# Kernel optimization log

Hardware: AMD Instinct MI355X
Metric: run time of the kernel (lower is better)

The kernel has to match this reference:

```python
import jax, jax.numpy as jnp
import numpy as np

CHUNK = 128


def selective_scan(x, A, Bm, Cm, dt, chunk_size):
    # x: [B,L,H,hd], Bm/Cm: [B,L,H,ds], A/dt: [H]. L must be divisible by chunk_size.
    Bb, L, H, hd = x.shape
    ds = Bm.shape[-1]
    cs = chunk_size
    nc = L // cs
    decay = jnp.exp(A * dt)  # [H]
    x_c = x.reshape(Bb, nc, cs, H, hd).transpose(0, 1, 3, 2, 4)   # [B,nc,H,cs,hd]
    B_c = Bm.reshape(Bb, nc, cs, H, ds).transpose(0, 1, 3, 2, 4)  # [B,nc,H,cs,ds]
    C_c = Cm.reshape(Bb, nc, cs, H, ds).transpose(0, 1, 3, 2, 4)
    x_dt = x_c * dt[None, None, :, None, None]
    idx = jnp.arange(cs, dtype=x.dtype)
    diff = idx[:, None] - idx[None, :]
    # causal intra-chunk decay matrix [H,cs,cs]
    L_mat = jnp.where(diff >= 0, decay[:, None, None] ** jnp.maximum(diff, 0.0), 0.0)
    CB = jnp.einsum('bnhid,bnhjd->bnhij', C_c, B_c)          # [B,nc,H,cs,cs]
    y_diag = jnp.einsum('bnhij,bnhjd->bnhid', CB * L_mat[None, None], x_dt)
    rev = jnp.arange(cs - 1, -1, -1, dtype=x.dtype)
    decay_rev = decay[:, None] ** rev[None, :]               # [H,cs]
    B_w = B_c * decay_rev[None, None, :, :, None]
    states = jnp.einsum('bnhjs,bnhjd->bnhsd', B_w, x_dt)     # [B,nc,H,ds,hd]
    cidx = jnp.arange(nc, dtype=x.dtype)
    shift = cidx[:, None] - cidx[None, :] - 1.0
    chunk_decay = decay ** cs
    M = jnp.where(shift >= 0, chunk_decay[:, None, None] ** jnp.maximum(shift, 0.0), 0.0)  # [H,nc,nc]
    h_carry = jnp.einsum('hij,bjhsd->bihsd', M, states)      # [B,nc,H,ds,hd]
    decay_out = decay[:, None] ** (idx[None, :] + 1.0)       # [H,cs]
    y_off = jnp.einsum('bnhis,bnhsd->bnhid', C_c, h_carry) * decay_out[None, None, :, :, None]
    y = (y_diag + y_off).transpose(0, 1, 3, 2, 4).reshape(Bb, L, H, hd)
    return y


def setup_inputs() -> dict:
    key = jax.random.key(0)
    ks = jax.random.split(key, 9)
    B, L, d_model, d_inner, H, ds, K = 2, 4096, 1024, 2048, 16, 128, 4
    s_dm = 1.0 / np.sqrt(d_model)
    s_di = 1.0 / np.sqrt(d_inner)
    x = jax.random.normal(ks[0], (B, L, d_model), jnp.float32)
    x_prenorm = jax.random.normal(ks[1], (B, L, d_model), jnp.float32)
    in_proj_w = jax.random.normal(ks[2], (2 * d_inner, d_model), jnp.float32) * s_dm
    conv_w = jax.random.normal(ks[3], (d_inner, 1, K), jnp.float32) * 0.5
    conv_b = jax.random.normal(ks[4], (d_inner,), jnp.float32) * 0.01
    B_proj_w = jax.random.normal(ks[5], (H * ds, d_model), jnp.float32) * s_dm
    C_proj_w = jax.random.normal(ks[6], (H * ds, d_model), jnp.float32) * s_dm
    dt_init = jax.random.uniform(ks[7], (H,), jnp.float32, 0.001, 0.1)
    dt_bias = dt_init + jnp.log(-jnp.expm1(-dt_init))  # inverse softplus
    A_log = jnp.log(jnp.arange(1, H + 1, dtype=jnp.float32))
    D_param = jnp.ones((H,), jnp.float32)
    out_proj_w = jax.random.normal(ks[8], (d_model, d_inner), jnp.float32) * s_di
    return dict(x=x, x_prenorm=x_prenorm, in_proj_w=in_proj_w, conv_w=conv_w,
                conv_b=conv_b, B_proj_w=B_proj_w, C_proj_w=C_proj_w,
                dt_bias=dt_bias, A_log=A_log, D_param=D_param, out_proj_w=out_proj_w)


def reference(x, x_prenorm, in_proj_w, conv_w, conv_b, B_proj_w, C_proj_w,
              dt_bias, A_log, D_param, out_proj_w):
    Bb, L, d_model = x.shape
    H = A_log.shape[0]
    ds = B_proj_w.shape[0] // H
    vg = x @ in_proj_w.T                        # [B,L,2*d_inner]
    d_inner = vg.shape[-1] // 2
    value, gate = vg[..., :d_inner], vg[..., d_inner:]
    K = conv_w.shape[-1]
    # causal depthwise conv1d (torch pads K-1 both sides then truncates right)
    v = jax.lax.conv_general_dilated(
        value.transpose(0, 2, 1), conv_w, (1,), [(K - 1, 0)],
        feature_group_count=d_inner, dimension_numbers=('NCH', 'OIH', 'NCH'))
    v = v + conv_b[None, :, None]
    value = jax.nn.silu(v.transpose(0, 2, 1))   # [B,L,d_inner]
    Bm = (x_prenorm @ B_proj_w.T).reshape(Bb, L, H, ds)
    Cm = (x_prenorm @ C_proj_w.T).reshape(Bb, L, H, ds)
    dt = jax.nn.softplus(dt_bias)
    A = -jnp.exp(A_log)
    hd = d_inner // H
    vh = value.reshape(Bb, L, H, hd)
    y = selective_scan(vh, A, Bm, Cm, dt, CHUNK)
    y = y + D_param[None, None, :, None] * vh
    y = y.reshape(Bb, L, d_inner) * jax.nn.silu(gate)
    return y @ out_proj_w.T
```

## Files before the change

kernel.cpp:

```cpp
#include <hip/hip_runtime.h>
#include <hip/hip_bf16.h>

#define NB 2
#define LSEQ 4096
#define DM 1024
#define DI 2048
#define NH 16
#define DSZ 128
#define CS 128
#define NCHUNK 32

using bf16 = __hip_bfloat16;
typedef __attribute__((ext_vector_type(8))) short short8;
typedef __attribute__((ext_vector_type(4))) float f32x4;

__device__ __forceinline__ float b2f(unsigned short u) {
    union { unsigned i; float f; } c; c.i = ((unsigned)u) << 16; return c.f;
}
__device__ __forceinline__ bf16 f2bf(float v) { return __float2bfloat16(v); }
__device__ __forceinline__ float bf2f(bf16 v) { return __bfloat162float(v); }

__device__ __forceinline__ float head_dt(const float* dt_bias, int h) {
    return log1pf(expf(dt_bias[h]));
}
__device__ __forceinline__ float head_l2dec(const float* dt_bias, const float* A_log, int h, float* dt_out) {
    float dt = head_dt(dt_bias, h);
    *dt_out = dt;
    return -expf(A_log[h]) * dt * 1.4426950408889634f;
}

__device__ __forceinline__ void storeC(bf16* C, size_t idx, float v) { C[idx] = f2bf(v); }
__device__ __forceinline__ void storeC(float* C, size_t idx, float v) { C[idx] = v; }

__device__ __forceinline__ void gload16(const bf16* g, bf16* l) {
    __builtin_amdgcn_global_load_lds(
        (const __attribute__((address_space(1))) void*)g,
        (__attribute__((address_space(3))) void*)l, 16, 0, 0);
}

__global__ __launch_bounds__(256) void cast_f2b(const float* __restrict__ in,
                                                bf16* __restrict__ out, long n) {
    long i = ((long)blockIdx.x * 256 + threadIdx.x) * 8;
    if (i >= n) return;
    float4 a = *reinterpret_cast<const float4*>(in + i);
    float4 b = *reinterpret_cast<const float4*>(in + i + 4);
    union { bf16 h[8]; short8 v; } o;
    o.h[0] = f2bf(a.x); o.h[1] = f2bf(a.y); o.h[2] = f2bf(a.z); o.h[3] = f2bf(a.w);
    o.h[4] = f2bf(b.x); o.h[5] = f2bf(b.y); o.h[6] = f2bf(b.z); o.h[7] = f2bf(b.w);
    *reinterpret_cast<short8*>(out + i) = o.v;
}

template <int MODE, typename TO>
__global__ __launch_bounds__(256) void gemm_mfma(const bf16* __restrict__ A,
                                                 const bf16* __restrict__ W,
                                                 TO* __restrict__ C0, TO* __restrict__ C1,
                                                 int N, int K) {
    __shared__ bf16 As[2][128 * 32];
    __shared__ bf16 Ws[2][128 * 32];
    const int tid = threadIdx.x;
    const int lane = tid & 63, w = tid >> 6;
    const int wr = w >> 1, wc = w & 1;
    const int bm = blockIdx.y * 128, bn = blockIdx.x * 128;
    const int srow = lane >> 2;
    const int skoff = (((lane & 3) ^ ((lane >> 2) & 3)) * 8);
    const int g0 = w * 2, g1 = w * 2 + 1;
    const int fr = lane & 15;
    const int fk = (((lane >> 4) ^ (lane & 3)) * 8);
    f32x4 acc[4][4] = {};
#define STAGE(buf, kt)                                                                  \
    do {                                                                                \
        gload16(A + (size_t)(bm + g0 * 16 + srow) * K + (kt) + skoff, &As[buf][g0 * 512]); \
        gload16(A + (size_t)(bm + g1 * 16 + srow) * K + (kt) + skoff, &As[buf][g1 * 512]); \
        gload16(W + (size_t)(bn + g0 * 16 + srow) * K + (kt) + skoff, &Ws[buf][g0 * 512]); \
        gload16(W + (size_t)(bn + g1 * 16 + srow) * K + (kt) + skoff, &Ws[buf][g1 * 512]); \
    } while (0)
    STAGE(0, 0);
    __syncthreads();
    const int NT = K / 32;
    int cur = 0;
    for (int t = 0; t < NT; ++t) {
        if (t + 1 < NT) STAGE(cur ^ 1, (t + 1) * 32);
        short8 af[4], bfr[4];
#pragma unroll
        for (int mi = 0; mi < 4; ++mi)
            af[mi] = *reinterpret_cast<const short8*>(&As[cur][(wr * 64 + mi * 16 + fr) * 32 + fk]);
#pragma unroll
        for (int ni = 0; ni < 4; ++ni)
            bfr[ni] = *reinterpret_cast<const short8*>(&Ws[cur][(wc * 64 + ni * 16 + fr) * 32 + fk]);
#pragma unroll
        for (int mi = 0; mi < 4; ++mi)
#pragma unroll
            for (int ni = 0; ni < 4; ++ni)
                acc[mi][ni] = __builtin_amdgcn_mfma_f32_16x16x32_bf16(af[mi], bfr[ni], acc[mi][ni], 0, 0, 0);
        __syncthreads();
        cur ^= 1;
    }
#undef STAGE
    const int orow0 = (lane >> 4) * 4;
    const int ocol = lane & 15;
#pragma unroll
    for (int mi = 0; mi < 4; ++mi)
#pragma unroll
        for (int ni = 0; ni < 4; ++ni) {
            int col = bn + wc * 64 + ni * 16 + ocol;
#pragma unroll
            for (int r = 0; r < 4; ++r) {
                int row = bm + wr * 64 + mi * 16 + orow0 + r;
                float v = acc[mi][ni][r];
                if (MODE == 1) {
                    if (col < DI) storeC(C0, (size_t)row * DI + col, v);
                    else          storeC(C1, (size_t)row * DI + (col - DI), v);
                } else {
                    storeC(C0, (size_t)row * N + col, v);
                }
            }
        }
}

__global__ __launch_bounds__(256) void conv_silu_vec(const bf16* __restrict__ vpre,
                                                     const float* __restrict__ cw,
                                                     const float* __restrict__ cb,
                                                     bf16* __restrict__ vpost) {
    size_t e = ((size_t)blockIdx.x * 256 + threadIdx.x) * 8;
    int c = (int)(e & (DI - 1));
    size_t bl = e >> 11;
    int l = (int)(bl & (LSEQ - 1));
    float vin[4][8];
#pragma unroll
    for (int k = 0; k < 4; ++k) {
        if (l - 3 + k >= 0) {
            short8 v = *reinterpret_cast<const short8*>(vpre + e + (long)(k - 3) * DI);
#pragma unroll
            for (int j = 0; j < 8; ++j) vin[k][j] = b2f((unsigned short)v[j]);
        } else {
#pragma unroll
            for (int j = 0; j < 8; ++j) vin[k][j] = 0.f;
        }
    }
    union { bf16 h[8]; short8 v; } o;
#pragma unroll
    for (int j = 0; j < 8; ++j) {
        float4 w4 = *reinterpret_cast<const float4*>(cw + (c + j) * 4);
        float s = cb[c + j] + w4.x * vin[0][j] + w4.y * vin[1][j] + w4.z * vin[2][j] + w4.w * vin[3][j];
        o.h[j] = f2bf(s / (1.f + expf(-s)));
    }
    *reinterpret_cast<short8*>(vpost + e) = o.v;
}

template <int SCALEMODE>
__global__ __launch_bounds__(256) void transpose_chunk(const bf16* __restrict__ in, bf16* __restrict__ outp,
                                                       const float* __restrict__ dt_bias,
                                                       const float* __restrict__ A_log) {
    __shared__ bf16 Ts[128][136];
    __shared__ float dpow[128];
    const int tid = threadIdx.x;
    const int bid = blockIdx.x;
    const int h = bid & 15, bn = bid >> 4;
    float dt; float l2d = head_l2dec(dt_bias, A_log, h, &dt);
    if (SCALEMODE == 1 && tid < 128) dpow[tid] = exp2f((float)(127 - tid) * l2d);
    const size_t base = (size_t)bn * CS * 2048 + (size_t)h * 128;
    {
        const int jr = tid >> 4, c8 = (tid & 15) * 8;
        for (int j0 = 0; j0 < 128; j0 += 16)
            *reinterpret_cast<short8*>(&Ts[j0 + jr][c8]) =
                *reinterpret_cast<const short8*>(in + base + (size_t)(j0 + jr) * 2048 + c8);
    }
    __syncthreads();
    const size_t ob = (size_t)bid * 16384;
    const int d = tid & 127;
    for (int jg = (tid >> 7); jg < 16; jg += 2) {
        int j0 = jg * 8;
        union { bf16 h8[8]; short8 v; } o;
#pragma unroll
        for (int e = 0; e < 8; ++e) {
            float val = bf2f(Ts[j0 + e][d]);
            val *= (SCALEMODE == 1) ? dpow[j0 + e] : dt;
            o.h8[e] = f2bf(val);
        }
        *reinterpret_cast<short8*>(outp + ob + (size_t)d * 128 + j0) = o.v;
    }
}

__global__ __launch_bounds__(256) void chunk_statesT(const bf16* __restrict__ XDT,
                                                     const bf16* __restrict__ BTg,
                                                     bf16* __restrict__ STT) {
    __shared__ bf16 XTs[128][72];
    __shared__ bf16 BTs[128][72];
    const int tid = threadIdx.x;
    const size_t ob = (size_t)blockIdx.x * 16384;
    const int lane = tid & 63, w = tid >> 6;
    const int fr = lane & 15, fk = (lane >> 4) * 8;
    f32x4 acc[2][8] = {};
    for (int j0 = 0; j0 < 128; j0 += 64) {
        for (int rr = 0; rr < 128; rr += 32) {
            int row = rr + (tid >> 3);
            int col = (tid & 7) * 8;
            *reinterpret_cast<short8*>(&XTs[row][col]) =
                *reinterpret_cast<const short8*>(XDT + ob + (size_t)row * 128 + j0 + col);
            *reinterpret_cast<short8*>(&BTs[row][col]) =
                *reinterpret_cast<const short8*>(BTg + ob + (size_t)row * 128 + j0 + col);
        }
        __syncthreads();
#pragma unroll
        for (int ks = 0; ks < 2; ++ks) {
            short8 a[2], bfr[8];
#pragma unroll
            for (int mi = 0; mi < 2; ++mi)
                a[mi] = *reinterpret_cast<const short8*>(&XTs[w * 32 + mi * 16 + fr][ks * 32 + fk]);
#pragma unroll
            for (int ni = 0; ni < 8; ++ni)
                bfr[ni] = *reinterpret_cast<const short8*>(&BTs[ni * 16 + fr][ks * 32 + fk]);
#pragma unroll
            for (int mi = 0; mi < 2; ++mi)
#pragma unroll
                for (int ni = 0; ni < 8; ++ni)
                    acc[mi][ni] = __builtin_amdgcn_mfma_f32_16x16x32_bf16(a[mi], bfr[ni], acc[mi][ni], 0, 0, 0);
        }
        __syncthreads();
    }
    const int orow0 = (lane >> 4) * 4, ocol = lane & 15;
#pragma unroll
    for (int mi = 0; mi < 2; ++mi)
#pragma unroll
        for (int ni = 0; ni < 8; ++ni) {
            int s = ni * 16 + ocol;
#pragma unroll
            for (int r = 0; r < 4; ++r) {
                int d = w * 32 + mi * 16 + orow0 + r;
                STT[ob + (size_t)d * 128 + s] = f2bf(acc[mi][ni][r]);
            }
        }
}

__global__ __launch_bounds__(256) void scan_kernel(bf16* __restrict__ ST,
                                                   const float* __restrict__ dt_bias,
                                                   const float* __restrict__ A_log) {
    const int q = blockIdx.x & 7;
    const int h = (blockIdx.x >> 3) & 15;
    const int b = blockIdx.x >> 7;
    float dt; float l2d = head_l2dec(dt_bias, A_log, h, &dt);
    float cd = exp2f(128.f * l2d);
    const int tid = threadIdx.x;
    float r[8] = {};
    for (int n = 0; n < NCHUNK; ++n) {
        size_t base = ((size_t)((b * NCHUNK + n) * NH + h)) * 16384 + (size_t)q * 2048;
#pragma unroll
        for (int e = 0; e < 8; ++e) {
            size_t idx = base + e * 256 + tid;
            float v = bf2f(ST[idx]);
            ST[idx] = f2bf(r[e]);
            r[e] = cd * r[e] + v;
        }
    }
}

__global__ __launch_bounds__(256) void chunk_cbl_mfma(const bf16* __restrict__ Bm, const bf16* __restrict__ Cm,
                                                      const float* __restrict__ dt_bias,
                                                      const float* __restrict__ A_log,
                                                      bf16* __restrict__ P) {
    __shared__ bf16 Cs[128][72];
    __shared__ bf16 Bs[128][72];
    const int tid = threadIdx.x;
    const int bid = blockIdx.x;
    const int h = bid & 15, bn = bid >> 4;
    float dt; float l2d = head_l2dec(dt_bias, A_log, h, &dt);
    const size_t base = (size_t)bn * CS * 2048 + (size_t)h * 128;
    const int lane = tid & 63, w = tid >> 6;
    const int fr = lane & 15, fk = (lane >> 4) * 8;
    f32x4 acc[2][8] = {};
    for (int s0 = 0; s0 < 128; s0 += 64) {
        for (int rr = 0; rr < 128; rr += 32) {
            int row = rr + (tid >> 3);
            int col = (tid & 7) * 8;
            *reinterpret_cast<short8*>(&Cs[row][col]) =
                *reinterpret_cast<const short8*>(Cm + base + (size_t)row * 2048 + s0 + col);
            *reinterpret_cast<short8*>(&Bs[row][col]) =
                *reinterpret_cast<const short8*>(Bm + base + (size_t)row * 2048 + s0 + col);
        }
        __syncthreads();
#pragma unroll
        for (int ks = 0; ks < 2; ++ks) {
            short8 a[2], bfr[8];
#pragma unroll
            for (int mi = 0; mi < 2; ++mi)
                a[mi] = *reinterpret_cast<const short8*>(&Cs[w * 32 + mi * 16 + fr][ks * 32 + fk]);
#pragma unroll
            for (int ni = 0; ni < 8; ++ni)
                bfr[ni] = *reinterpret_cast<const short8*>(&Bs[ni * 16 + fr][ks * 32 + fk]);
#pragma unroll
            for (int mi = 0; mi < 2; ++mi)
#pragma unroll
                for (int ni = 0; ni < 8; ++ni)
                    acc[mi][ni] = __builtin_amdgcn_mfma_f32_16x16x32_bf16(a[mi], bfr[ni], acc[mi][ni], 0, 0, 0);
        }
        __syncthreads();
    }
    const size_t ob = (size_t)bid * 16384;
    const int orow0 = (lane >> 4) * 4, ocol = lane & 15;
#pragma unroll
    for (int mi = 0; mi < 2; ++mi)
#pragma unroll
        for (int ni = 0; ni < 8; ++ni) {
            int j = ni * 16 + ocol;
#pragma unroll
            for (int r = 0; r < 4; ++r) {
                int i = w * 32 + mi * 16 + orow0 + r;
                float v = (i >= j) ? acc[mi][ni][r] * exp2f((float)(i - j) * l2d) : 0.f;
                P[ob + (size_t)i * 128 + j] = f2bf(v);
            }
        }
}

__global__ __launch_bounds__(256) void chunk_y_mfma(const bf16* __restrict__ P, const bf16* __restrict__ Cm,
                                                    const bf16* __restrict__ STT, const bf16* __restrict__ XDT,
                                                    const float* __restrict__ dt_bias,
                                                    const float* __restrict__ A_log,
                                                    const float* __restrict__ D_param,
                                                    bf16* __restrict__ gateY) {
    __shared__ bf16 Ps[128][72];
    __shared__ bf16 XTs[128][72];
    const int tid = threadIdx.x;
    const int bid = blockIdx.x;
    const int h = bid & 15, bn = bid >> 4;
    float dt; float l2d = head_l2dec(dt_bias, A_log, h, &dt);
    const size_t base = (size_t)bn * CS * 2048 + (size_t)h * 128;
    const size_t ob = (size_t)bid * 16384;
    const int lane = tid & 63, w = tid >> 6;
    const int fr = lane & 15, fk = (lane >> 4) * 8;
    const int orow0 = (lane >> 4) * 4, ocol = lane & 15;
    f32x4 acc[2][8] = {};
#pragma unroll
    for (int ks = 0; ks < 4; ++ks) {
        short8 a[2], bfr[8];
#pragma unroll
        for (int mi = 0; mi < 2; ++mi)
            a[mi] = *reinterpret_cast<const short8*>(Cm + base + (size_t)(w * 32 + mi * 16 + fr) * 2048 + ks * 32 + fk);
#pragma unroll
        for (int ni = 0; ni < 8; ++ni)
            bfr[ni] = *reinterpret_cast<const short8*>(STT + ob + (size_t)(ni * 16 + fr) * 128 + ks * 32 + fk);
#pragma unroll
        for (int mi = 0; mi < 2; ++mi)
#pragma unroll
            for (int ni = 0; ni < 8; ++ni)
                acc[mi][ni] = __builtin_amdgcn_mfma_f32_16x16x32_bf16(a[mi], bfr[ni], acc[mi][ni], 0, 0, 0);
    }
#pragma unroll
    for (int mi = 0; mi < 2; ++mi)
#pragma unroll
        for (int r = 0; r < 4; ++r) {
            int i = w * 32 + mi * 16 + orow0 + r;
            float sc = exp2f((float)(i + 1) * l2d);
#pragma unroll
            for (int ni = 0; ni < 8; ++ni) acc[mi][ni][r] *= sc;
        }
    for (int j0 = 0; j0 < 128; j0 += 64) {
        for (int rr = 0; rr < 128; rr += 32) {
            int row = rr + (tid >> 3);
            int col = (tid & 7) * 8;
            *reinterpret_cast<short8*>(&Ps[row][col]) =
                *reinterpret_cast<const short8*>(P + ob + (size_t)row * 128 + j0 + col);
            *reinterpret_cast<short8*>(&XTs[row][col]) =
                *reinterpret_cast<const short8*>(XDT + ob + (size_t)row * 128 + j0 + col);
        }
        __syncthreads();
#pragma unroll
        for (int ks = 0; ks < 2; ++ks) {
            short8 a[2], bfr[8];
#pragma unroll
            for (int mi = 0; mi < 2; ++mi)
                a[mi] = *reinterpret_cast<const short8*>(&Ps[w * 32 + mi * 16 + fr][ks * 32 + fk]);
#pragma unroll
            for (int ni = 0; ni < 8; ++ni)
                bfr[ni] = *reinterpret_cast<const short8*>(&XTs[ni * 16 + fr][ks * 32 + fk]);
#pragma unroll
            for (int mi = 0; mi < 2; ++mi)
#pragma unroll
                for (int ni = 0; ni < 8; ++ni)
                    acc[mi][ni] = __builtin_amdgcn_mfma_f32_16x16x32_bf16(a[mi], bfr[ni], acc[mi][ni], 0, 0, 0);
        }
        __syncthreads();
    }
    const float Dv = D_param[h];
    const float inv_dt = 1.f / dt;
#pragma unroll
    for (int mi = 0; mi < 2; ++mi)
#pragma unroll
        for (int ni = 0; ni < 8; ++ni) {
            int d = ni * 16 + ocol;
#pragma unroll
            for (int r = 0; r < 4; ++r) {
                int i = w * 32 + mi * 16 + orow0 + r;
                size_t idx = base + (size_t)i * 2048 + d;
                float v = bf2f(XDT[ob + (size_t)d * 128 + i]) * inv_dt;
                float yv = acc[mi][ni][r] + Dv * v;
                float g = bf2f(gateY[idx]);
                gateY[idx] = f2bf(yv * g / (1.f + expf(-g)));
            }
        }
}

extern "C" void kernel_launch(void* const* d_in, const int* in_sizes, int n_in,
                              void* d_out, int out_size, void* d_ws, size_t ws_size,
                              hipStream_t stream) {
    (void)out_size;
    static const int exp_sizes[11] = {
        NB * LSEQ * DM, NB * LSEQ * DM, 2 * DI * DM, DI * 4, DI,
        NH * DSZ * DM, NH * DSZ * DM, NH, NH, NH, DM * DI
    };
    if (n_in != 11) return;
    for (int i = 0; i < 11; ++i) if (in_sizes[i] != exp_sizes[i]) return;

    const float* x         = (const float*)d_in[0];
    const float* x_prenorm = (const float*)d_in[1];
    const float* in_proj_w = (const float*)d_in[2];
    const float* conv_w    = (const float*)d_in[3];
    const float* conv_b    = (const float*)d_in[4];
    const float* B_proj_w  = (const float*)d_in[5];
    const float* C_proj_w  = (const float*)d_in[6];
    const float* dt_bias   = (const float*)d_in[7];
    const float* A_log     = (const float*)d_in[8];
    const float* D_param   = (const float*)d_in[9];
    const float* out_proj_w= (const float*)d_in[10];
    float* out = (float*)d_out;

    const size_t NE = (size_t)NB * LSEQ * DI;
    const size_t SLOT = NE * 2;
    if (ws_size < 5 * SLOT) return;
    char* ws = (char*)d_ws;
    bf16* S0 = (bf16*)(ws);
    bf16* S1 = (bf16*)(ws + SLOT);
    bf16* S2 = (bf16*)(ws + 2 * SLOT);
    bf16* S3 = (bf16*)(ws + 3 * SLOT);
    bf16* S4 = (bf16*)(ws + 4 * SLOT);

    bf16* xb   = (bf16*)d_out;
    bf16* wBCb = (bf16*)((char*)d_out + 16777216);
    bf16* wIb = S3;
    bf16* wOb = S3;
    bf16* BTg = (bf16*)d_out;
    bf16* Pbuf = (bf16*)d_out;

    const int M = NB * LSEQ;
    const int NC = NB * NCHUNK * NH;
    dim3 blk(256);

    cast_f2b<<<dim3(4096), blk, 0, stream>>>(x, xb, (long)NB * LSEQ * DM);
    cast_f2b<<<dim3(2048), blk, 0, stream>>>(in_proj_w, wIb, (long)2 * DI * DM);
    gemm_mfma<1, bf16><<<dim3(2 * DI / 128, M / 128), blk, 0, stream>>>(xb, wIb, S0, S1, 2 * DI, DM);
    conv_silu_vec<<<dim3((unsigned)(NE / 2048)), blk, 0, stream>>>(S0, conv_w, conv_b, S2);
    cast_f2b<<<dim3(4096), blk, 0, stream>>>(x_prenorm, xb, (long)NB * LSEQ * DM);
    cast_f2b<<<dim3(1024), blk, 0, stream>>>(B_proj_w, wBCb, (long)NH * DSZ * DM);
    cast_f2b<<<dim3(1024), blk, 0, stream>>>(C_proj_w, wBCb + (size_t)NH * DSZ * DM, (long)NH * DSZ * DM);
    gemm_mfma<1, bf16><<<dim3(2 * DI / 128, M / 128), blk, 0, stream>>>(xb, wBCb, S3, S4, 2 * DI, DM);
    transpose_chunk<0><<<dim3(NC), blk, 0, stream>>>(S2, S0, dt_bias, A_log);
    transpose_chunk<1><<<dim3(NC), blk, 0, stream>>>(S3, BTg, dt_bias, A_log);
    chunk_statesT<<<dim3(NC), blk, 0, stream>>>(S0, BTg, S2);
    scan_kernel<<<dim3(NB * NH * 8), blk, 0, stream>>>(S2, dt_bias, A_log);
    chunk_cbl_mfma<<<dim3(NC), blk, 0, stream>>>(S3, S4, dt_bias, A_log, Pbuf);
    chunk_y_mfma<<<dim3(NC), blk, 0, stream>>>(Pbuf, S4, S2, S0, dt_bias, A_log, D_param, S1);
    cast_f2b<<<dim3(1024), blk, 0, stream>>>(out_proj_w, wOb, (long)DM * DI);
    gemm_mfma<2, float><<<dim3(DM / 128, M / 128), blk, 0, stream>>>(S1, wOb, out, nullptr, DM, DI);
}
```

Baseline: 437.0 us.

## Use 256x256-tile 512-thread MFMA GEMM for input and B/C projections

Adds a larger GEMM kernel with 256x256 output tiles, 8 waves each computing a 128x64 sub-tile, and double-buffered direct-to-LDS loads. It replaces the 128x128 GEMM for the two 8192x4096x1024 projection GEMMs. The larger tiles raise arithmetic intensity and cut global/L2 traffic per FLOP. The cost is much higher register pressure (128 accumulator floats per thread) and a smaller grid of 256 blocks, which may limit occupancy on a 256-CU device.

```diff
diff --git a/kernel.cpp b/kernel.cpp
--- a/kernel.cpp
+++ b/kernel.cpp
@@ -48,6 +48,89 @@
     o.h[0] = f2bf(a.x); o.h[1] = f2bf(a.y); o.h[2] = f2bf(a.z); o.h[3] = f2bf(a.w);
     o.h[4] = f2bf(b.x); o.h[5] = f2bf(b.y); o.h[6] = f2bf(b.z); o.h[7] = f2bf(b.w);
     *reinterpret_cast<short8*>(out + i) = o.v;
+}
+
+template <int MODE, typename TO>
+__global__ __launch_bounds__(512, 2) void gemm_big(const bf16* __restrict__ A,
+                                                   const bf16* __restrict__ W,
+                                                   TO* __restrict__ C0, TO* __restrict__ C1,
+                                                   int N, int K) {
+    __shared__ bf16 As[2][256 * 32];
+    __shared__ bf16 Ws[2][256 * 32];
+    const int tid = threadIdx.x;
+    const int lane = tid & 63, w = tid >> 6;
+    const int wm = w >> 2, wn = w & 3;
+    const int bm = blockIdx.y * 256, bn = blockIdx.x * 256;
+    const int srow = lane >> 2;
+    const int skoff = ((lane & 3) ^ ((lane >> 2) & 3)) * 8;
+    const int fr = lane & 15, fq = lane >> 4;
+    f32x4 acc[8][4] = {};
+
+#define STAGE(buf, kt)                                                                        \
+    do {                                                                                      \
+        gload16(A + (size_t)(bm + w * 32 + srow) * K + (kt) + skoff, &As[buf][(w * 32) * 32]);       \
+        gload16(A + (size_t)(bm + w * 32 + 16 + srow) * K + (kt) + skoff, &As[buf][(w * 32 + 16) * 32]); \
+        gload16(W + (size_t)(bn + w * 32 + srow) * K + (kt) + skoff, &Ws[buf][(w * 32) * 32]);       \
+        gload16(W + (size_t)(bn + w * 32 + 16 + srow) * K + (kt) + skoff, &Ws[buf][(w * 32 + 16) * 32]); \
+    } while (0)
+
+    const int NT = K / 32;
+    STAGE(0, 0);
+    STAGE(1, 32);
+    asm volatile("s_waitcnt vmcnt(4)" ::: "memory");
+    __builtin_amdgcn_s_barrier();
+
+    for (int t = 0; t < NT; ++t) {
+        const int buf = t & 1;
+        short8 bfrag[4];
+#pragma unroll
+        for (int n = 0; n < 4; ++n) {
+            int brow = wn * 64 + n * 16 + fr;
+            bfrag[n] = *reinterpret_cast<const short8*>(&Ws[buf][brow * 32 + ((fq ^ (fr & 3)) << 3)]);
+        }
+#pragma unroll
+        for (int m = 0; m < 8; ++m) {
+            int arow = wm * 128 + m * 16 + fr;
+            short8 af = *reinterpret_cast<const short8*>(&As[buf][arow * 32 + ((fq ^ (fr & 3)) << 3)]);
+#pragma unroll
+            for (int n = 0; n < 4; ++n)
+                acc[m][n] = __builtin_amdgcn_mfma_f32_16x16x32_bf16(af, bfrag[n], acc[m][n], 0, 0, 0);
+        }
+        if (t == NT - 1) break;
+        __builtin_amdgcn_sched_barrier(0);
+        asm volatile("s_waitcnt lgkmcnt(0)" ::: "memory");
+        __builtin_amdgcn_sched_barrier(0);
+        __builtin_amdgcn_s_barrier();
+        if (t + 2 < NT) {
+            STAGE(buf, (t + 2) * 32);
+            asm volatile("s_waitcnt vmcnt(4)" ::: "memory");
+        } else {
+            asm volatile("s_waitcnt vmcnt(0)" ::: "memory");
+        }
+        __builtin_amdgcn_sched_barrier(0);
+        __builtin_amdgcn_s_barrier();
+    }
+#undef STAGE
+
+    const int orow0 = (lane >> 4) * 4;
+    const int ocol = lane & 15;
+#pragma unroll
+    for (int m = 0; m < 8; ++m)
+#pragma unroll
+        for (int n = 0; n < 4; ++n) {
+            int col = bn + wn * 64 + n * 16 + ocol;
+#pragma unroll
+            for (int r = 0; r < 4; ++r) {
+                int row = bm + wm * 128 + m * 16 + orow0 + r;
+                float v = acc[m][n][r];
+                if (MODE == 1) {
+                    if (col < DI) storeC(C0, (size_t)row * DI + col, v);
+                    else          storeC(C1, (size_t)row * DI + (col - DI), v);
+                } else {
+                    storeC(C0, (size_t)row * N + col, v);
+                }
+            }
+        }
 }
 
 template <int MODE, typename TO>
@@ -443,15 +526,16 @@
     const int M = NB * LSEQ;
     const int NC = NB * NCHUNK * NH;
     dim3 blk(256);
+    dim3 blk512(512);
 
     cast_f2b<<<dim3(4096), blk, 0, stream>>>(x, xb, (long)NB * LSEQ * DM);
     cast_f2b<<<dim3(2048), blk, 0, stream>>>(in_proj_w, wIb, (long)2 * DI * DM);
-    gemm_mfma<1, bf16><<<dim3(2 * DI / 128, M / 128), blk, 0, stream>>>(xb, wIb, S0, S1, 2 * DI, DM);
+    gemm_big<1, bf16><<<dim3(2 * DI / 256, M / 256), blk512, 0, stream>>>(xb, wIb, S0, S1, 2 * DI, DM);
     conv_silu_vec<<<dim3((unsigned)(NE / 2048)), blk, 0, stream>>>(S0, conv_w, conv_b, S2);
     cast_f2b<<<dim3(4096), blk, 0, stream>>>(x_prenorm, xb, (long)NB * LSEQ * DM);
     cast_f2b<<<dim3(1024), blk, 0, stream>>>(B_proj_w, wBCb, (long)NH * DSZ * DM);
     cast_f2b<<<dim3(1024), blk, 0, stream>>>(C_proj_w, wBCb + (size_t)NH * DSZ * DM, (long)NH * DSZ * DM);
-    gemm_mfma<1, bf16><<<dim3(2 * DI / 128, M / 128), blk, 0, stream>>>(xb, wBCb, S3, S4, 2 * DI, DM);
+    gemm_big<1, bf16><<<dim3(2 * DI / 256, M / 256), blk512, 0, stream>>>(xb, wBCb, S3, S4, 2 * DI, DM);
     transpose_chunk<0><<<dim3(NC), blk, 0, stream>>>(S2, S0, dt_bias, A_log);
     transpose_chunk<1><<<dim3(NC), blk, 0, stream>>>(S3, BTg, dt_bias, A_log);
     chunk_statesT<<<dim3(NC), blk, 0, stream>>>(S0, BTg, S2);
```

Measured after the change: 454.3 us. 4.0% more time.

## Fuse conv+transpose, emit decayed B transpose from GEMM, merge CB and Y kernels

Applied to the files above, without the earlier changes.

Merges the depthwise conv/SiLU with the dt-scaled chunk transpose into one kernel. The B/C projection GEMM epilogue now also writes the decay-weighted, transposed B chunk, so the separate transpose kernel goes away. The CB·L kernel and the chunk-output kernel are combined so the masked P matrix stays in shared memory instead of going through global memory. This removes several launches and intermediate round-trips, but the GEMM epilogue now does scattered, uncoalesced bf16 stores and chunk_statesT writes in place over its B input.

```diff
diff --git a/kernel.cpp b/kernel.cpp
--- a/kernel.cpp
+++ b/kernel.cpp
@@ -54,6 +54,8 @@
 __global__ __launch_bounds__(256) void gemm_mfma(const bf16* __restrict__ A,
                                                  const bf16* __restrict__ W,
                                                  TO* __restrict__ C0, TO* __restrict__ C1,
+                                                 bf16* __restrict__ C2,
+                                                 const float* dt_bias, const float* A_log,
                                                  int N, int K) {
     __shared__ bf16 As[2][128 * 32];
     __shared__ bf16 Ws[2][128 * 32];
@@ -103,13 +105,26 @@
 #pragma unroll
         for (int ni = 0; ni < 4; ++ni) {
             int col = bn + wc * 64 + ni * 16 + ocol;
+            float l2d = 0.f;
+            if (MODE == 3 && col < DI) {
+                float dtq;
+                l2d = head_l2dec(dt_bias, A_log, (col >> 7) & 15, &dtq);
+            }
 #pragma unroll
             for (int r = 0; r < 4; ++r) {
                 int row = bm + wr * 64 + mi * 16 + orow0 + r;
                 float v = acc[mi][ni][r];
-                if (MODE == 1) {
-                    if (col < DI) storeC(C0, (size_t)row * DI + col, v);
-                    else          storeC(C1, (size_t)row * DI + (col - DI), v);
+                if (MODE == 1 || MODE == 3) {
+                    if (col < DI) {
+                        storeC(C0, (size_t)row * DI + col, v);
+                        if (MODE == 3) {
+                            int j = row & 127, s = col & 127;
+                            size_t btb = ((size_t)(blockIdx.y * 16 + ((col >> 7) & 15))) * 16384;
+                            C2[btb + (size_t)s * 128 + j] = f2bf(v * exp2f((float)(127 - j) * l2d));
+                        }
+                    } else {
+                        storeC(C1, (size_t)row * DI + (col - DI), v);
+                    }
                 } else {
                     storeC(C0, (size_t)row * N + col, v);
                 }
@@ -117,73 +132,72 @@
         }
 }
 
-__global__ __launch_bounds__(256) void conv_silu_vec(const bf16* __restrict__ vpre,
-                                                     const float* __restrict__ cw,
-                                                     const float* __restrict__ cb,
-                                                     bf16* __restrict__ vpost) {
-    size_t e = ((size_t)blockIdx.x * 256 + threadIdx.x) * 8;
-    int c = (int)(e & (DI - 1));
-    size_t bl = e >> 11;
-    int l = (int)(bl & (LSEQ - 1));
-    float vin[4][8];
-#pragma unroll
-    for (int k = 0; k < 4; ++k) {
-        if (l - 3 + k >= 0) {
-            short8 v = *reinterpret_cast<const short8*>(vpre + e + (long)(k - 3) * DI);
-#pragma unroll
-            for (int j = 0; j < 8; ++j) vin[k][j] = b2f((unsigned short)v[j]);
-        } else {
-#pragma unroll
-            for (int j = 0; j < 8; ++j) vin[k][j] = 0.f;
-        }
-    }
-    union { bf16 h[8]; short8 v; } o;
-#pragma unroll
-    for (int j = 0; j < 8; ++j) {
-        float4 w4 = *reinterpret_cast<const float4*>(cw + (c + j) * 4);
-        float s = cb[c + j] + w4.x * vin[0][j] + w4.y * vin[1][j] + w4.z * vin[2][j] + w4.w * vin[3][j];
-        o.h[j] = f2bf(s / (1.f + expf(-s)));
-    }
-    *reinterpret_cast<short8*>(vpost + e) = o.v;
-}
-
-template <int SCALEMODE>
-__global__ __launch_bounds__(256) void transpose_chunk(const bf16* __restrict__ in, bf16* __restrict__ outp,
-                                                       const float* __restrict__ dt_bias,
-                                                       const float* __restrict__ A_log) {
-    __shared__ bf16 Ts[128][136];
-    __shared__ float dpow[128];
+__global__ __launch_bounds__(256) void conv_xdt(const bf16* __restrict__ vpre,
+                                                const float* __restrict__ cw,
+                                                const float* __restrict__ cb,
+                                                const float* __restrict__ dt_bias,
+                                                bf16* __restrict__ XDT) {
+    __shared__ bf16 Ts[131][136];
+    __shared__ bf16 T2[128][136];
+    __shared__ float wks[128][4];
+    __shared__ float cbs[128];
     const int tid = threadIdx.x;
     const int bid = blockIdx.x;
-    const int h = bid & 15, bn = bid >> 4;
-    float dt; float l2d = head_l2dec(dt_bias, A_log, h, &dt);
-    if (SCALEMODE == 1 && tid < 128) dpow[tid] = exp2f((float)(127 - tid) * l2d);
-    const size_t base = (size_t)bn * CS * 2048 + (size_t)h * 128;
+    const int h = bid & 15, g = bid >> 4;
+    const int n31 = g & 31;
+    const float dt = head_dt(dt_bias, h);
+    if (tid < 128) {
+        float4 w4 = *reinterpret_cast<const float4*>(cw + (h * 128 + tid) * 4);
+        wks[tid][0] = w4.x; wks[tid][1] = w4.y; wks[tid][2] = w4.z; wks[tid][3] = w4.w;
+        cbs[tid] = cb[h * 128 + tid];
+    }
     {
-        const int jr = tid >> 4, c8 = (tid & 15) * 8;
-        for (int j0 = 0; j0 < 128; j0 += 16)
-            *reinterpret_cast<short8*>(&Ts[j0 + jr][c8]) =
-                *reinterpret_cast<const short8*>(in + base + (size_t)(j0 + jr) * 2048 + c8);
+        const int lr = tid >> 4, c8 = (tid & 15) * 8;
+        for (int i0 = 0; i0 < 144; i0 += 16) {
+            int i = i0 + lr;
+            if (i < 131) {
+                short8 v = {0, 0, 0, 0, 0, 0, 0, 0};
+                if (!(n31 == 0 && i < 3))
+                    v = *reinterpret_cast<const short8*>(vpre + (size_t)(g * 128 - 3 + i) * 2048 + h * 128 + c8);
+                *reinterpret_cast<short8*>(&Ts[i][c8]) = v;
+            }
+        }
     }
     __syncthreads();
-    const size_t ob = (size_t)bid * 16384;
-    const int d = tid & 127;
-    for (int jg = (tid >> 7); jg < 16; jg += 2) {
-        int j0 = jg * 8;
-        union { bf16 h8[8]; short8 v; } o;
-#pragma unroll
-        for (int e = 0; e < 8; ++e) {
-            float val = bf2f(Ts[j0 + e][d]);
-            val *= (SCALEMODE == 1) ? dpow[j0 + e] : dt;
-            o.h8[e] = f2bf(val);
-        }
-        *reinterpret_cast<short8*>(outp + ob + (size_t)d * 128 + j0) = o.v;
+    {
+        const int jr = tid >> 4, d8 = (tid & 15) * 8;
+        for (int j0 = 0; j0 < 128; j0 += 16) {
+            int j = j0 + jr;
+            union { bf16 hh[8]; short8 v; } o;
+#pragma unroll
+            for (int e = 0; e < 8; ++e) {
+                int d = d8 + e;
+                float s = cbs[d];
+#pragma unroll
+                for (int k = 0; k < 4; ++k) s += wks[d][k] * bf2f(Ts[j + k][d]);
+                float sil = s / (1.f + expf(-s));
+                o.hh[e] = f2bf(sil * dt);
+            }
+            *reinterpret_cast<short8*>(&T2[j][d8]) = o.v;
+        }
+    }
+    __syncthreads();
+    {
+        const size_t ob = (size_t)bid * 16384;
+        const int d = tid & 127;
+        for (int jg = (tid >> 7); jg < 16; jg += 2) {
+            int j0 = jg * 8;
+            union { bf16 hh[8]; short8 v; } o;
+#pragma unroll
+            for (int e = 0; e < 8; ++e) o.hh[e] = T2[j0 + e][d];
+            *reinterpret_cast<short8*>(XDT + ob + (size_t)d * 128 + j0) = o.v;
+        }
     }
 }
 
 __global__ __launch_bounds__(256) void chunk_statesT(const bf16* __restrict__ XDT,
-                                                     const bf16* __restrict__ BTg,
-                                                     bf16* __restrict__ STT) {
+                                                     const bf16* BTg,
+                                                     bf16* STT) {
     __shared__ bf16 XTs[128][72];
     __shared__ bf16 BTs[128][72];
     const int tid = threadIdx.x;
@@ -254,80 +268,67 @@
     }
 }
 
-__global__ __launch_bounds__(256) void chunk_cbl_mfma(const bf16* __restrict__ Bm, const bf16* __restrict__ Cm,
-                                                      const float* __restrict__ dt_bias,
-                                                      const float* __restrict__ A_log,
-                                                      bf16* __restrict__ P) {
-    __shared__ bf16 Cs[128][72];
-    __shared__ bf16 Bs[128][72];
+__global__ __launch_bounds__(256) void chunk_cbl_y(const bf16* __restrict__ Bm, const bf16* __restrict__ Cm,
+                                                   const bf16* __restrict__ STT, const bf16* __restrict__ XDT,
+                                                   const float* __restrict__ dt_bias,
+                                                   const float* __restrict__ A_log,
+                                                   const float* __restrict__ D_param,
+                                                   bf16* __restrict__ gateY) {
+    __shared__ bf16 T1[128][72];
+    __shared__ bf16 T2[128][72];
+    __shared__ bf16 Ps[128][136];
     const int tid = threadIdx.x;
     const int bid = blockIdx.x;
-    const int h = bid & 15, bn = bid >> 4;
+    const int h = bid & 15, g = bid >> 4;
     float dt; float l2d = head_l2dec(dt_bias, A_log, h, &dt);
-    const size_t base = (size_t)bn * CS * 2048 + (size_t)h * 128;
-    const int lane = tid & 63, w = tid >> 6;
-    const int fr = lane & 15, fk = (lane >> 4) * 8;
-    f32x4 acc[2][8] = {};
-    for (int s0 = 0; s0 < 128; s0 += 64) {
-        for (int rr = 0; rr < 128; rr += 32) {
-            int row = rr + (tid >> 3);
-            int col = (tid & 7) * 8;
-            *reinterpret_cast<short8*>(&Cs[row][col]) =
-                *reinterpret_cast<const short8*>(Cm + base + (size_t)row * 2048 + s0 + col);
-            *reinterpret_cast<short8*>(&Bs[row][col]) =
-                *reinterpret_cast<const short8*>(Bm + base + (size_t)row * 2048 + s0 + col);
-        }
-        __syncthreads();
-#pragma unroll
-        for (int ks = 0; ks < 2; ++ks) {
-            short8 a[2], bfr[8];
-#pragma unroll
-            for (int mi = 0; mi < 2; ++mi)
-                a[mi] = *reinterpret_cast<const short8*>(&Cs[w * 32 + mi * 16 + fr][ks * 32 + fk]);
-#pragma unroll
-            for (int ni = 0; ni < 8; ++ni)
-                bfr[ni] = *reinterpret_cast<const short8*>(&Bs[ni * 16 + fr][ks * 32 + fk]);
-#pragma unroll
-            for (int mi = 0; mi < 2; ++mi)
-#pragma unroll
-                for (int ni = 0; ni < 8; ++ni)
-                    acc[mi][ni] = __builtin_amdgcn_mfma_f32_16x16x32_bf16(a[mi], bfr[ni], acc[mi][ni], 0, 0, 0);
-        }
-        __syncthreads();
-    }
-    const size_t ob = (size_t)bid * 16384;
-    const int orow0 = (lane >> 4) * 4, ocol = lane & 15;
-#pragma unroll
-    for (int mi = 0; mi < 2; ++mi)
-#pragma unroll
-        for (int ni = 0; ni < 8; ++ni) {
-            int j = ni * 16 + ocol;
-#pragma unroll
-            for (int r = 0; r < 4; ++r) {
-                int i = w * 32 + mi * 16 + orow0 + r;
-                float v = (i >= j) ? acc[mi][ni][r] * exp2f((float)(i - j) * l2d) : 0.f;
-                P[ob + (size_t)i * 128 + j] = f2bf(v);
-            }
-        }
-}
-
-__global__ __launch_bounds__(256) void chunk_y_mfma(const bf16* __restrict__ P, const bf16* __restrict__ Cm,
-                                                    const bf16* __restrict__ STT, const bf16* __restrict__ XDT,
-                                                    const float* __restrict__ dt_bias,
-                                                    const float* __restrict__ A_log,
-                                                    const float* __restrict__ D_param,
-                                                    bf16* __restrict__ gateY) {
-    __shared__ bf16 Ps[128][72];
-    __shared__ bf16 XTs[128][72];
-    const int tid = threadIdx.x;
-    const int bid = blockIdx.x;
-    const int h = bid & 15, bn = bid >> 4;
-    float dt; float l2d = head_l2dec(dt_bias, A_log, h, &dt);
-    const size_t base = (size_t)bn * CS * 2048 + (size_t)h * 128;
+    const size_t base = (size_t)g * CS * 2048 + (size_t)h * 128;
     const size_t ob = (size_t)bid * 16384;
     const int lane = tid & 63, w = tid >> 6;
     const int fr = lane & 15, fk = (lane >> 4) * 8;
     const int orow0 = (lane >> 4) * 4, ocol = lane & 15;
+    {
+        f32x4 pacc[2][8] = {};
+        for (int s0 = 0; s0 < 128; s0 += 64) {
+            for (int rr = 0; rr < 128; rr += 32) {
+                int row = rr + (tid >> 3);
+                int col = (tid & 7) * 8;
+                *reinterpret_cast<short8*>(&T1[row][col]) =
+                    *reinterpret_cast<const short8*>(Cm + base + (size_t)row * 2048 + s0 + col);
+                *reinterpret_cast<short8*>(&T2[row][col]) =
+                    *reinterpret_cast<const short8*>(Bm + base + (size_t)row * 2048 + s0 + col);
+            }
+            __syncthreads();
+#pragma unroll
+            for (int ks = 0; ks < 2; ++ks) {
+                short8 a[2], bfr[8];
+#pragma unroll
+                for (int mi = 0; mi < 2; ++mi)
+                    a[mi] = *reinterpret_cast<const short8*>(&T1[w * 32 + mi * 16 + fr][ks * 32 + fk]);
+#pragma unroll
+                for (int ni = 0; ni < 8; ++ni)
+                    bfr[ni] = *reinterpret_cast<const short8*>(&T2[ni * 16 + fr][ks * 32 + fk]);
+#pragma unroll
+                for (int mi = 0; mi < 2; ++mi)
+#pragma unroll
+                    for (int ni = 0; ni < 8; ++ni)
+                        pacc[mi][ni] = __builtin_amdgcn_mfma_f32_16x16x32_bf16(a[mi], bfr[ni], pacc[mi][ni], 0, 0, 0);
+            }
+            __syncthreads();
+        }
+#pragma unroll
+        for (int mi = 0; mi < 2; ++mi)
+#pragma unroll
+            for (int ni = 0; ni < 8; ++ni) {
+                int j = ni * 16 + ocol;
+#pragma unroll
+                for (int r = 0; r < 4; ++r) {
+                    int i = w * 32 + mi * 16 + orow0 + r;
+                    float v = (i >= j) ? pacc[mi][ni][r] * exp2f((float)(i - j) * l2d) : 0.f;
+                    Ps[i][j] = f2bf(v);
+                }
+            }
+    }
+    __syncthreads();
     f32x4 acc[2][8] = {};
 #pragma unroll
     for (int ks = 0; ks < 4; ++ks) {
@@ -357,9 +358,7 @@
         for (int rr = 0; rr < 128; rr += 32) {
             int row = rr + (tid >> 3);
             int col = (tid & 7) * 8;
-            *reinterpret_cast<short8*>(&Ps[row][col]) =
-                *reinterpret_cast<const short8*>(P + ob + (size_t)row * 128 + j0 + col);
-            *reinterpret_cast<short8*>(&XTs[row][col]) =
+            *reinterpret_cast<short8*>(&T1[row][col]) =
                 *reinterpret_cast<const short8*>(XDT + ob + (size_t)row * 128 + j0 + col);
         }
         __syncthreads();
@@ -368,10 +367,10 @@
             short8 a[2], bfr[8];
 #pragma unroll
             for (int mi = 0; mi < 2; ++mi)
-                a[mi] = *reinterpret_cast<const short8*>(&Ps[w * 32 + mi * 16 + fr][ks * 32 + fk]);
+                a[mi] = *reinterpret_cast<const short8*>(&Ps[w * 32 + mi * 16 + fr][j0 + ks * 32 + fk]);
 #pragma unroll
             for (int ni = 0; ni < 8; ++ni)
-                bfr[ni] = *reinterpret_cast<const short8*>(&XTs[ni * 16 + fr][ks * 32 + fk]);
+                bfr[ni] = *reinterpret_cast<const short8*>(&T1[ni * 16 + fr][ks * 32 + fk]);
 #pragma unroll
             for (int mi = 0; mi < 2; ++mi)
 #pragma unroll
@@ -393,8 +392,8 @@
                 size_t idx = base + (size_t)i * 2048 + d;
                 float v = bf2f(XDT[ob + (size_t)d * 128 + i]) * inv_dt;
                 float yv = acc[mi][ni][r] + Dv * v;
-                float g = bf2f(gateY[idx]);
-                gateY[idx] = f2bf(yv * g / (1.f + expf(-g)));
+                float gq = bf2f(gateY[idx]);
+                gateY[idx] = f2bf(yv * gq / (1.f + expf(-gq)));
             }
         }
 }
@@ -435,29 +434,25 @@
 
     bf16* xb   = (bf16*)d_out;
     bf16* wBCb = (bf16*)((char*)d_out + 16777216);
-    bf16* wIb = S3;
-    bf16* wOb = S3;
-    bf16* BTg = (bf16*)d_out;
-    bf16* Pbuf = (bf16*)d_out;
 
     const int M = NB * LSEQ;
     const int NC = NB * NCHUNK * NH;
     dim3 blk(256);
 
     cast_f2b<<<dim3(4096), blk, 0, stream>>>(x, xb, (long)NB * LSEQ * DM);
-    cast_f2b<<<dim3(2048), blk, 0, stream>>>(in_proj_w, wIb, (long)2 * DI * DM);
-    gemm_mfma<1, bf16><<<dim3(2 * DI / 128, M / 128), blk, 0, stream>>>(xb, wIb, S0, S1, 2 * DI, DM);
-    conv_silu_vec<<<dim3((unsigned)(NE / 2048)), blk, 0, stream>>>(S0, conv_w, conv_b, S2);
+    cast_f2b<<<dim3(2048), blk, 0, stream>>>(in_proj_w, S3, (long)2 * DI * DM);
+    gemm_mfma<1, bf16><<<dim3(2 * DI / 128, M / 128), blk, 0, stream>>>(
+        xb, S3, S0, S1, nullptr, nullptr, nullptr, 2 * DI, DM);
+    conv_xdt<<<dim3(NC), blk, 0, stream>>>(S0, conv_w, conv_b, dt_bias, S2);
     cast_f2b<<<dim3(4096), blk, 0, stream>>>(x_prenorm, xb, (long)NB * LSEQ * DM);
     cast_f2b<<<dim3(1024), blk, 0, stream>>>(B_proj_w, wBCb, (long)NH * DSZ * DM);
     cast_f2b<<<dim3(1024), blk, 0, stream>>>(C_proj_w, wBCb + (size_t)NH * DSZ * DM, (long)NH * DSZ * DM);
-    gemm_mfma<1, bf16><<<dim3(2 * DI / 128, M / 128), blk, 0, stream>>>(xb, wBCb, S3, S4, 2 * DI, DM);
-    transpose_chunk<0><<<dim3(NC), blk, 0, stream>>>(S2, S0, dt_bias, A_log);
-    transpose_chunk<1><<<dim3(NC), blk, 0, stream>>>(S3, BTg, dt_bias, A_log);
-    chunk_statesT<<<dim3(NC), blk, 0, stream>>>(S0, BTg, S2);
-    scan_kernel<<<dim3(NB * NH * 8), blk, 0, stream>>>(S2, dt_bias, A_log);
-    chunk_cbl_mfma<<<dim3(NC), blk, 0, stream>>>(S3, S4, dt_bias, A_log, Pbuf);
-    chunk_y_mfma<<<dim3(NC), blk, 0, stream>>>(Pbuf, S4, S2, S0, dt_bias, A_log, D_param, S1);
-    cast_f2b<<<dim3(1024), blk, 0, stream>>>(out_proj_w, wOb, (long)DM * DI);
-    gemm_mfma<2, float><<<dim3(DM / 128, M / 128), blk, 0, stream>>>(S1, wOb, out, nullptr, DM, DI);
-}
+    gemm_mfma<3, bf16><<<dim3(2 * DI / 128, M / 128), blk, 0, stream>>>(
+        xb, wBCb, S3, S4, S0, dt_bias, A_log, 2 * DI, DM);
+    chunk_statesT<<<dim3(NC), blk, 0, stream>>>(S2, S0, S0);
+    scan_kernel<<<dim3(NB * NH * 8), blk, 0, stream>>>(S0, dt_bias, A_log);
+    chunk_cbl_y<<<dim3(NC), blk, 0, stream>>>(S3, S4, S0, S2, dt_bias, A_log, D_param, S1);
+    cast_f2b<<<dim3(1024), blk, 0, stream>>>(out_proj_w, S3, (long)DM * DI);
+    gemm_mfma<2, float><<<dim3(DM / 128, M / 128), blk, 0, stream>>>(
+        S1, S3, out, nullptr, nullptr, nullptr, nullptr, DM, DI);
+}
```

Result: slower. 521.2 us (+19.3%).
